# Kernel tuning notes

Measured on AMD Instinct MI355X. Metric: run time of the kernel, lower is better.

The kernel has to match this reference:

```python
import jax, jax.numpy as jnp
import numpy as np

N, IN_F, OUT_F, K = 256, 1024, 128, 32

def setup_inputs() -> dict:
    key = jax.random.key(0)
    k1, k2 = jax.random.split(key)
    x = jax.random.normal(k1, (N, IN_F), dtype=jnp.float32)
    T = jax.random.normal(k2, (IN_F, OUT_F, K), dtype=jnp.float32)
    return {"x": x, "T": T}

def reference(x, T):
    # matrices: [N, OUT_F, K]
    M = jnp.einsum('ni,iok->nok', x, T)
    # pairwise L1 distance over kernel dim: [N, N, OUT_F]
    norm = jnp.abs(M[:, None, :, :] - M[None, :, :, :]).sum(axis=3)
    expnorm = jnp.exp(-norm)
    # sum over the other-sample axis; subtract self-term exp(0)=1
    o_b = expnorm.sum(axis=0) - 1.0  # [N, OUT_F]
    return jnp.concatenate([x, o_b], axis=1)
```

## Files before the change

### kernel.cpp

```cpp
#include <hip/hip_runtime.h>

typedef unsigned short u16;
typedef __attribute__((ext_vector_type(8))) short short8_t;
typedef __attribute__((ext_vector_type(4))) float f32x4;

#define N_SAMP 256
#define IN_F   1024
#define OUT_F  128
#define KDIM   32
#define JTOT   (OUT_F * KDIM)
#define OUT_ROW (IN_F + OUT_F)

#define CHUNKS 8
#define MPC    32
#define MPW    8

__device__ __forceinline__ u16 f2bf(float f) {
    union { float f; unsigned u; } v; v.f = f;
    unsigned r = v.u + 0x7FFFu + ((v.u >> 16) & 1u);
    return (u16)(r >> 16);
}


__global__ __launch_bounds__(256) void copy_init_conv(const float* __restrict__ x,
                                                      float* __restrict__ out,
                                                      u16* __restrict__ At) {
    int n = blockIdx.x, t = threadIdx.x;
    float4 v = reinterpret_cast<const float4*>(x + (size_t)n * IN_F)[t];
    reinterpret_cast<float4*>(out + (size_t)n * OUT_ROW)[t] = v;
    ushort4 b;
    b.x = f2bf(v.x); b.y = f2bf(v.y); b.z = f2bf(v.z); b.w = f2bf(v.w);
    reinterpret_cast<ushort4*>(At + (size_t)n * IN_F)[t] = b;
}

__global__ __launch_bounds__(256) void convT_kernel(const float* __restrict__ T,
                                                    u16* __restrict__ Bt) {
    __shared__ float Ls[64 * 65];
    const int t = threadIdx.x;
    const int j0 = blockIdx.x * 64, k0 = blockIdx.y * 64;
    const int r = t >> 2, c4 = t & 3;

    const float4* src = reinterpret_cast<const float4*>(T + (size_t)(k0 + r) * JTOT + j0 + c4 * 16);
    float4 v0 = src[0], v1 = src[1], v2 = src[2], v3 = src[3];
    float vv[16] = {v0.x,v0.y,v0.z,v0.w, v1.x,v1.y,v1.z,v1.w,
                    v2.x,v2.y,v2.z,v2.w, v3.x,v3.y,v3.z,v3.w};
#pragma unroll
    for (int i = 0; i < 16; ++i) Ls[r * 65 + c4 * 16 + i] = vv[i];
    __syncthreads();

    unsigned pk[8];
#pragma unroll
    for (int i = 0; i < 8; ++i) {
        u16 lo = f2bf(Ls[(c4 * 16 + 2 * i    ) * 65 + r]);
        u16 hi = f2bf(Ls[(c4 * 16 + 2 * i + 1) * 65 + r]);
        pk[i] = (unsigned)lo | ((unsigned)hi << 16);
    }
    uint4* dst = reinterpret_cast<uint4*>(Bt + (size_t)(j0 + r) * IN_F + k0 + c4 * 16);
    dst[0] = make_uint4(pk[0], pk[1], pk[2], pk[3]);
    dst[1] = make_uint4(pk[4], pk[5], pk[6], pk[7]);
}

#define LDB 136
__global__ __launch_bounds__(128) void mfma_gemm(const u16* __restrict__ At,
                                                 const u16* __restrict__ Bt,
                                                 float* __restrict__ Mt) {
    __shared__ u16 Bs[64 * LDB];
    __shared__ u16 As[32 * LDB];
    const int t = threadIdx.x;
    const int w = t >> 6, l = t & 63;
    const int jb = blockIdx.x * 64, nb = blockIdx.y * 32;
    const int rb = t >> 1, hb = t & 1;
    const int ra = t >> 2, qa = t & 3;

    f32x4 acc00 = {0.f,0.f,0.f,0.f}, acc01 = {0.f,0.f,0.f,0.f};
    f32x4 acc10 = {0.f,0.f,0.f,0.f}, acc11 = {0.f,0.f,0.f,0.f};

    float4 sb[8], sa[4];
    auto LOADG = [&](int it) {
        const float4* gb = reinterpret_cast<const float4*>(Bt + (size_t)(jb + rb) * IN_F + it * 128 + hb * 64);
#pragma unroll
        for (int i = 0; i < 8; ++i) sb[i] = gb[i];
        const float4* ga = reinterpret_cast<const float4*>(At + (size_t)(nb + ra) * IN_F + it * 128 + qa * 32);
#pragma unroll
        for (int i = 0; i < 4; ++i) sa[i] = ga[i];
    };
    auto STORE = [&]() {
#pragma unroll
        for (int i = 0; i < 8; ++i) *reinterpret_cast<float4*>(&Bs[rb * LDB + hb * 64 + i * 8]) = sb[i];
#pragma unroll
        for (int i = 0; i < 4; ++i) *reinterpret_cast<float4*>(&As[ra * LDB + qa * 32 + i * 8]) = sa[i];
    };

    LOADG(0); STORE(); __syncthreads();

    for (int it = 0; it < 8; ++it) {
        if (it < 7) LOADG(it + 1);
#pragma unroll
        for (int s = 0; s < 4; ++s) {
            const int co = s * 32 + 8 * (l >> 4);
            short8_t a0 = *reinterpret_cast<const short8_t*>(&Bs[(w * 32 +      (l & 15)) * LDB + co]);
            short8_t a1 = *reinterpret_cast<const short8_t*>(&Bs[(w * 32 + 16 + (l & 15)) * LDB + co]);
            short8_t b0 = *reinterpret_cast<const short8_t*>(&As[(          (l & 15)) * LDB + co]);
            short8_t b1 = *reinterpret_cast<const short8_t*>(&As[(     16 + (l & 15)) * LDB + co]);
            acc00 = __builtin_amdgcn_mfma_f32_16x16x32_bf16(a0, b0, acc00, 0, 0, 0);
            acc01 = __builtin_amdgcn_mfma_f32_16x16x32_bf16(a0, b1, acc01, 0, 0, 0);
            acc10 = __builtin_amdgcn_mfma_f32_16x16x32_bf16(a1, b0, acc10, 0, 0, 0);
            acc11 = __builtin_amdgcn_mfma_f32_16x16x32_bf16(a1, b1, acc11, 0, 0, 0);
        }
        __syncthreads();
        if (it < 7) { STORE(); __syncthreads(); }
    }

    const int jrow = jb + w * 32 + (l >> 4) * 4;
    const int ncol = nb + (l & 15);
#pragma unroll
    for (int r = 0; r < 4; ++r) {
        Mt[(size_t)(jrow + r     ) * N_SAMP + ncol     ] = acc00[r];
        Mt[(size_t)(jrow + r     ) * N_SAMP + ncol + 16] = acc01[r];
        Mt[(size_t)(jrow + 16 + r) * N_SAMP + ncol     ] = acc10[r];
        Mt[(size_t)(jrow + 16 + r) * N_SAMP + ncol + 16] = acc11[r];
    }
}

__global__ __launch_bounds__(256) void dist_part(const float* __restrict__ Mt,
                                                 float* __restrict__ part) {
    __shared__ float Mo[MPC][36];
    __shared__ float Pred[4][N_SAMP];
    const int t = threadIdx.x, w = t >> 6, l = t & 63;
    const int o  = blockIdx.x;
    const int mb = blockIdx.y * MPC;

    {
        const int m = t & 31, kb = (t >> 5) * 4;
#pragma unroll
        for (int kk = 0; kk < 4; ++kk)
            Mo[m][kb + kk] = Mt[(size_t)(o * KDIM + kb + kk) * N_SAMP + mb + m];
    }
    __syncthreads();

    float accd[4][MPW];
#pragma unroll
    for (int r = 0; r < 4; ++r)
#pragma unroll
        for (int m = 0; m < MPW; ++m) accd[r][m] = 0.f;

#pragma unroll
    for (int kh = 0; kh < 4; ++kh) {
        float r0[8], r1[8], r2[8], r3[8];
#pragma unroll
        for (int k = 0; k < 8; ++k) {
            const float* p = Mt + (size_t)(o * KDIM + kh * 8 + k) * N_SAMP + l;
            r0[k] = p[0]; r1[k] = p[64]; r2[k] = p[128]; r3[k] = p[192];
        }
#pragma unroll
        for (int m = 0; m < MPW; ++m) {
            float mo[8];
#pragma unroll
            for (int i = 0; i < 2; ++i)
                *reinterpret_cast<float4*>(&mo[i * 4]) =
                    *reinterpret_cast<const float4*>(&Mo[w * MPW + m][kh * 8 + i * 4]);
#pragma unroll
            for (int k = 0; k < 8; ++k) {
                accd[0][m] += fabsf(r0[k] - mo[k]);
                accd[1][m] += fabsf(r1[k] - mo[k]);
                accd[2][m] += fabsf(r2[k] - mo[k]);
                accd[3][m] += fabsf(r3[k] - mo[k]);
            }
        }
    }

    float a0 = 0.f, a1 = 0.f, a2 = 0.f, a3 = 0.f;
#pragma unroll
    for (int m = 0; m < MPW; ++m) {
        a0 += __expf(-accd[0][m]); a1 += __expf(-accd[1][m]);
        a2 += __expf(-accd[2][m]); a3 += __expf(-accd[3][m]);
    }
    Pred[w][l] = a0; Pred[w][l + 64] = a1; Pred[w][l + 128] = a2; Pred[w][l + 192] = a3;
    __syncthreads();

    {
        float s = Pred[0][t] + Pred[1][t] + Pred[2][t] + Pred[3][t];
        part[(size_t)blockIdx.y * (OUT_F * N_SAMP) + o * N_SAMP + t] = s;
    }
}

__global__ __launch_bounds__(128) void dist_reduce(const float* __restrict__ part,
                                                   float* __restrict__ out) {
    const int n = blockIdx.x, t = threadIdx.x;
    float s = -1.0f;
#pragma unroll
    for (int c = 0; c < CHUNKS; ++c)
        s += part[(size_t)c * (OUT_F * N_SAMP) + t * N_SAMP + n];
    out[(size_t)n * OUT_ROW + IN_F + t] = s;
}

__global__ __launch_bounds__(256) void copy_init_kernel(const float* __restrict__ x,
                                                        float* __restrict__ out) {
    int n = blockIdx.x, t = threadIdx.x;
    reinterpret_cast<float4*>(out + (size_t)n * OUT_ROW)[t] =
        reinterpret_cast<const float4*>(x + (size_t)n * IN_F)[t];
    if (t < OUT_F) out[(size_t)n * OUT_ROW + IN_F + t] = -1.0f;
}

#define BM 64
#define BN 64
#define BK 16
#define AS_STRIDE 68
__global__ __launch_bounds__(256) void gemm_kernel(const float* __restrict__ x,
                                                   const float* __restrict__ T,
                                                   float* __restrict__ M) {
    __shared__ float As_[BK][AS_STRIDE];
    __shared__ float Bs_[BK][BN];
    const int jb = blockIdx.x * BN, nb = blockIdx.y * BM;
    const int t = threadIdx.x, tx = t & 15, ty = t >> 4;
    float acc[4][4] = {};
    for (int k0 = 0; k0 < IN_F; k0 += BK) {
        {
            int row = t >> 2, cg = (t & 3) * 4;
            float4 v = *reinterpret_cast<const float4*>(&x[(size_t)(nb + row) * IN_F + k0 + cg]);
            As_[cg + 0][row] = v.x; As_[cg + 1][row] = v.y;
            As_[cg + 2][row] = v.z; As_[cg + 3][row] = v.w;
        }
        {
            int r = t >> 4, cg = (t & 15) * 4;
            *reinterpret_cast<float4*>(&Bs_[r][cg]) =
                *reinterpret_cast<const float4*>(&T[(size_t)(k0 + r) * JTOT + jb + cg]);
        }
        __syncthreads();
#pragma unroll
        for (int kk = 0; kk < BK; ++kk) {
            float4 av = *reinterpret_cast<const float4*>(&As_[kk][ty * 4]);
            float4 bv = *reinterpret_cast<const float4*>(&Bs_[kk][tx * 4]);
            float a[4] = {av.x, av.y, av.z, av.w}, b[4] = {bv.x, bv.y, bv.z, bv.w};
#pragma unroll
            for (int i = 0; i < 4; ++i)
#pragma unroll
                for (int j = 0; j < 4; ++j) acc[i][j] += a[i] * b[j];
        }
        __syncthreads();
    }
#pragma unroll
    for (int i = 0; i < 4; ++i) {
        int n = nb + ty * 4 + i;
        float4 v = make_float4(acc[i][0], acc[i][1], acc[i][2], acc[i][3]);
        *reinterpret_cast<float4*>(&M[(size_t)n * JTOT + jb + tx * 4]) = v;
    }
}

__global__ __launch_bounds__(256) void dist_kernel(const float* __restrict__ M,
                                                   float* __restrict__ out) {
    __shared__ float Mo_[64][KDIM];
    const int o = blockIdx.x >> 2, chunk = blockIdx.x & 3, t = threadIdx.x;
    float r[KDIM];
    const float4* mrow = reinterpret_cast<const float4*>(&M[(size_t)t * JTOT + o * KDIM]);
#pragma unroll
    for (int f = 0; f < 8; ++f) {
        float4 v = mrow[f];
        r[f*4+0]=v.x; r[f*4+1]=v.y; r[f*4+2]=v.z; r[f*4+3]=v.w;
    }
    const int mbase = chunk * 64;
    {
        int row = t >> 3, f4 = t & 7;
        *reinterpret_cast<float4*>(&Mo_[row][f4*4]) =
            *reinterpret_cast<const float4*>(&M[(size_t)(mbase+row)*JTOT + o*KDIM + f4*4]);
        *reinterpret_cast<float4*>(&Mo_[row+32][f4*4]) =
            *reinterpret_cast<const float4*>(&M[(size_t)(mbase+row+32)*JTOT + o*KDIM + f4*4]);
    }
    __syncthreads();
    float acc = 0.f;
    for (int m = 0; m < 64; ++m) {
        float d = 0.f;
#pragma unroll
        for (int k = 0; k < KDIM; ++k) d += fabsf(r[k] - Mo_[m][k]);
        acc += __expf(-d);
    }
    atomicAdd(&out[(size_t)t * OUT_ROW + IN_F + o], acc);
}

extern "C" void kernel_launch(void* const* d_in, const int* in_sizes, int n_in,
                              void* d_out, int out_size, void* d_ws, size_t ws_size,
                              hipStream_t stream) {
    const float* x = (const float*)d_in[0];
    const float* T = (const float*)d_in[1];
    float* out = (float*)d_out;

    const size_t MT_BYTES = (size_t)JTOT * N_SAMP * 4;
    const size_t AT_BYTES = (size_t)N_SAMP * IN_F * 2;
    const size_t BT_BYTES = (size_t)JTOT * IN_F * 2;

    if (ws_size >= MT_BYTES + AT_BYTES + BT_BYTES) {
        float* Mt = (float*)d_ws;
        u16*   At = (u16*)((char*)d_ws + MT_BYTES);
        u16*   Bt = (u16*)((char*)d_ws + MT_BYTES + AT_BYTES);
        float* part = (float*)Bt;

        copy_init_conv<<<N_SAMP, 256, 0, stream>>>(x, out, At);
        convT_kernel<<<dim3(JTOT / 64, IN_F / 64), 256, 0, stream>>>(T, Bt);
        mfma_gemm<<<dim3(JTOT / 64, N_SAMP / 32), 128, 0, stream>>>(At, Bt, Mt);
        dist_part<<<dim3(OUT_F, CHUNKS), 256, 0, stream>>>(Mt, part);
        dist_reduce<<<N_SAMP, 128, 0, stream>>>(part, out);
    } else {
        float* M = (float*)d_ws;
        copy_init_kernel<<<N_SAMP, 256, 0, stream>>>(x, out);
        dim3 ggrid(JTOT / BN, N_SAMP / BM);
        gemm_kernel<<<ggrid, 256, 0, stream>>>(x, T, M);
        dist_kernel<<<OUT_F * 4, 256, 0, stream>>>(M, out);
    }
}
```

Measured before the change: 120.5 us.

## Fuse GEMM and pairwise L1 distance per output feature into one kernel

Replaces the separate T transpose/convert, MFMA GEMM and distance-partial kernels with one fused kernel per (output feature, half of samples). Each block converts its 32-column slice of T to bf16 on the fly with double buffering, computes all 256 samples' M rows with MFMA, keeps them in shared memory, then computes L1 distances and exp sums directly. This removes the Mt and Bt round trips through global memory and two launches. In exchange the GEMM is computed twice, once per half-block, and A is read straight from global memory without LDS staging. The grid is only 256 blocks of 512 threads, which may limit occupancy.

```diff
diff --git a/kernel.cpp b/kernel.cpp
--- a/kernel.cpp
+++ b/kernel.cpp
@@ -11,20 +11,22 @@
 #define JTOT   (OUT_F * KDIM)
 #define OUT_ROW (IN_F + OUT_F)
 
-#define CHUNKS 8
-#define MPC    32
-#define MPW    8
+#define LDBS 72
+#define LDMS 36
 
 __device__ __forceinline__ u16 f2bf(float f) {
     union { float f; unsigned u; } v; v.f = f;
     unsigned r = v.u + 0x7FFFu + ((v.u >> 16) & 1u);
     return (u16)(r >> 16);
 }
-
-
-__global__ __launch_bounds__(256) void copy_init_conv(const float* __restrict__ x,
-                                                      float* __restrict__ out,
-                                                      u16* __restrict__ At) {
+__device__ __forceinline__ unsigned pack2(float lo, float hi) {
+    return (unsigned)f2bf(lo) | ((unsigned)f2bf(hi) << 16);
+}
+
+
+__global__ __launch_bounds__(256) void conv_x(const float* __restrict__ x,
+                                              float* __restrict__ out,
+                                              u16* __restrict__ At) {
     int n = blockIdx.x, t = threadIdx.x;
     float4 v = reinterpret_cast<const float4*>(x + (size_t)n * IN_F)[t];
     reinterpret_cast<float4*>(out + (size_t)n * OUT_ROW)[t] = v;
@@ -33,165 +35,134 @@
     reinterpret_cast<ushort4*>(At + (size_t)n * IN_F)[t] = b;
 }
 
-__global__ __launch_bounds__(256) void convT_kernel(const float* __restrict__ T,
-                                                    u16* __restrict__ Bt) {
-    __shared__ float Ls[64 * 65];
-    const int t = threadIdx.x;
-    const int j0 = blockIdx.x * 64, k0 = blockIdx.y * 64;
-    const int r = t >> 2, c4 = t & 3;
-
-    const float4* src = reinterpret_cast<const float4*>(T + (size_t)(k0 + r) * JTOT + j0 + c4 * 16);
-    float4 v0 = src[0], v1 = src[1], v2 = src[2], v3 = src[3];
-    float vv[16] = {v0.x,v0.y,v0.z,v0.w, v1.x,v1.y,v1.z,v1.w,
-                    v2.x,v2.y,v2.z,v2.w, v3.x,v3.y,v3.z,v3.w};
-#pragma unroll
-    for (int i = 0; i < 16; ++i) Ls[r * 65 + c4 * 16 + i] = vv[i];
+__global__ __launch_bounds__(512) void fused_od(const u16* __restrict__ At,
+                                                const float* __restrict__ T,
+                                                float* __restrict__ part) {
+    __shared__ u16   Bs[2][32 * LDBS];
+    __shared__ float Ms[N_SAMP * LDMS];
+    __shared__ float Pred[8][N_SAMP];
+    const int t = threadIdx.x, w = t >> 6, l = t & 63;
+    const int o  = blockIdx.x >> 1;
+    const int mh = blockIdx.x & 1;
+    const int jb = o * KDIM;
+
+    const int jt = t & 7, kp = t >> 3;
+    float4 ta, tb;
+    auto LOADT = [&](int c) {
+        if (t < 256) {
+            const int k0 = c * 64;
+            ta = *reinterpret_cast<const float4*>(&T[(size_t)(k0 + 2 * kp    ) * JTOT + jb + jt * 4]);
+            tb = *reinterpret_cast<const float4*>(&T[(size_t)(k0 + 2 * kp + 1) * JTOT + jb + jt * 4]);
+        }
+    };
+    auto STORET = [&](int b) {
+        if (t < 256) {
+            const float* fa = reinterpret_cast<const float*>(&ta);
+            const float* fb = reinterpret_cast<const float*>(&tb);
+#pragma unroll
+            for (int c = 0; c < 4; ++c)
+                *reinterpret_cast<unsigned*>(&Bs[b][(jt * 4 + c) * LDBS + 2 * kp]) = pack2(fa[c], fb[c]);
+        }
+    };
+
+    f32x4 acc[2][2];
+#pragma unroll
+    for (int a = 0; a < 2; ++a)
+#pragma unroll
+        for (int b = 0; b < 2; ++b) acc[a][b] = (f32x4){0.f, 0.f, 0.f, 0.f};
+
+    LOADT(0); STORET(0); __syncthreads();
+
+    for (int c = 0; c < 16; ++c) {
+        const int cur = c & 1;
+        if (c < 15) LOADT(c + 1);
+        const u16* at0 = &At[(size_t)(w * 32 +      (l & 15)) * IN_F + c * 64];
+        const u16* at1 = &At[(size_t)(w * 32 + 16 + (l & 15)) * IN_F + c * 64];
+#pragma unroll
+        for (int s = 0; s < 2; ++s) {
+            const int co = s * 32 + 8 * (l >> 4);
+            short8_t a0 = *reinterpret_cast<const short8_t*>(&Bs[cur][(     (l & 15)) * LDBS + co]);
+            short8_t a1 = *reinterpret_cast<const short8_t*>(&Bs[cur][(16 + (l & 15)) * LDBS + co]);
+            short8_t b0 = *reinterpret_cast<const short8_t*>(&at0[co]);
+            short8_t b1 = *reinterpret_cast<const short8_t*>(&at1[co]);
+            acc[0][0] = __builtin_amdgcn_mfma_f32_16x16x32_bf16(a0, b0, acc[0][0], 0, 0, 0);
+            acc[0][1] = __builtin_amdgcn_mfma_f32_16x16x32_bf16(a0, b1, acc[0][1], 0, 0, 0);
+            acc[1][0] = __builtin_amdgcn_mfma_f32_16x16x32_bf16(a1, b0, acc[1][0], 0, 0, 0);
+            acc[1][1] = __builtin_amdgcn_mfma_f32_16x16x32_bf16(a1, b1, acc[1][1], 0, 0, 0);
+        }
+        if (c < 15) STORET(cur ^ 1);
+        __syncthreads();
+    }
+
+#pragma unroll
+    for (int jt2 = 0; jt2 < 2; ++jt2)
+#pragma unroll
+        for (int nt = 0; nt < 2; ++nt) {
+            const int n  = w * 32 + nt * 16 + (l & 15);
+            const int j0 = jt2 * 16 + (l >> 4) * 4;
+#pragma unroll
+            for (int r = 0; r < 4; ++r)
+                Ms[n * LDMS + j0 + r] = acc[jt2][nt][r];
+        }
     __syncthreads();
 
-    unsigned pk[8];
-#pragma unroll
-    for (int i = 0; i < 8; ++i) {
-        u16 lo = f2bf(Ls[(c4 * 16 + 2 * i    ) * 65 + r]);
-        u16 hi = f2bf(Ls[(c4 * 16 + 2 * i + 1) * 65 + r]);
-        pk[i] = (unsigned)lo | ((unsigned)hi << 16);
-    }
-    uint4* dst = reinterpret_cast<uint4*>(Bt + (size_t)(j0 + r) * IN_F + k0 + c4 * 16);
-    dst[0] = make_uint4(pk[0], pk[1], pk[2], pk[3]);
-    dst[1] = make_uint4(pk[4], pk[5], pk[6], pk[7]);
-}
-
-#define LDB 136
-__global__ __launch_bounds__(128) void mfma_gemm(const u16* __restrict__ At,
-                                                 const u16* __restrict__ Bt,
-                                                 float* __restrict__ Mt) {
-    __shared__ u16 Bs[64 * LDB];
-    __shared__ u16 As[32 * LDB];
-    const int t = threadIdx.x;
-    const int w = t >> 6, l = t & 63;
-    const int jb = blockIdx.x * 64, nb = blockIdx.y * 32;
-    const int rb = t >> 1, hb = t & 1;
-    const int ra = t >> 2, qa = t & 3;
-
-    f32x4 acc00 = {0.f,0.f,0.f,0.f}, acc01 = {0.f,0.f,0.f,0.f};
-    f32x4 acc10 = {0.f,0.f,0.f,0.f}, acc11 = {0.f,0.f,0.f,0.f};
-
-    float4 sb[8], sa[4];
-    auto LOADG = [&](int it) {
-        const float4* gb = reinterpret_cast<const float4*>(Bt + (size_t)(jb + rb) * IN_F + it * 128 + hb * 64);
-#pragma unroll
-        for (int i = 0; i < 8; ++i) sb[i] = gb[i];
-        const float4* ga = reinterpret_cast<const float4*>(At + (size_t)(nb + ra) * IN_F + it * 128 + qa * 32);
-#pragma unroll
-        for (int i = 0; i < 4; ++i) sa[i] = ga[i];
-    };
-    auto STORE = [&]() {
-#pragma unroll
-        for (int i = 0; i < 8; ++i) *reinterpret_cast<float4*>(&Bs[rb * LDB + hb * 64 + i * 8]) = sb[i];
-#pragma unroll
-        for (int i = 0; i < 4; ++i) *reinterpret_cast<float4*>(&As[ra * LDB + qa * 32 + i * 8]) = sa[i];
-    };
-
-    LOADG(0); STORE(); __syncthreads();
-
-    for (int it = 0; it < 8; ++it) {
-        if (it < 7) LOADG(it + 1);
-#pragma unroll
-        for (int s = 0; s < 4; ++s) {
-            const int co = s * 32 + 8 * (l >> 4);
-            short8_t a0 = *reinterpret_cast<const short8_t*>(&Bs[(w * 32 +      (l & 15)) * LDB + co]);
-            short8_t a1 = *reinterpret_cast<const short8_t*>(&Bs[(w * 32 + 16 + (l & 15)) * LDB + co]);
-            short8_t b0 = *reinterpret_cast<const short8_t*>(&As[(          (l & 15)) * LDB + co]);
-            short8_t b1 = *reinterpret_cast<const short8_t*>(&As[(     16 + (l & 15)) * LDB + co]);
-            acc00 = __builtin_amdgcn_mfma_f32_16x16x32_bf16(a0, b0, acc00, 0, 0, 0);
-            acc01 = __builtin_amdgcn_mfma_f32_16x16x32_bf16(a0, b1, acc01, 0, 0, 0);
-            acc10 = __builtin_amdgcn_mfma_f32_16x16x32_bf16(a1, b0, acc10, 0, 0, 0);
-            acc11 = __builtin_amdgcn_mfma_f32_16x16x32_bf16(a1, b1, acc11, 0, 0, 0);
-        }
-        __syncthreads();
-        if (it < 7) { STORE(); __syncthreads(); }
-    }
-
-    const int jrow = jb + w * 32 + (l >> 4) * 4;
-    const int ncol = nb + (l & 15);
-#pragma unroll
-    for (int r = 0; r < 4; ++r) {
-        Mt[(size_t)(jrow + r     ) * N_SAMP + ncol     ] = acc00[r];
-        Mt[(size_t)(jrow + r     ) * N_SAMP + ncol + 16] = acc01[r];
-        Mt[(size_t)(jrow + 16 + r) * N_SAMP + ncol     ] = acc10[r];
-        Mt[(size_t)(jrow + 16 + r) * N_SAMP + ncol + 16] = acc11[r];
-    }
-}
-
-__global__ __launch_bounds__(256) void dist_part(const float* __restrict__ Mt,
-                                                 float* __restrict__ part) {
-    __shared__ float Mo[MPC][36];
-    __shared__ float Pred[4][N_SAMP];
-    const int t = threadIdx.x, w = t >> 6, l = t & 63;
-    const int o  = blockIdx.x;
-    const int mb = blockIdx.y * MPC;
-
-    {
-        const int m = t & 31, kb = (t >> 5) * 4;
-#pragma unroll
-        for (int kk = 0; kk < 4; ++kk)
-            Mo[m][kb + kk] = Mt[(size_t)(o * KDIM + kb + kk) * N_SAMP + mb + m];
-    }
-    __syncthreads();
-
-    float accd[4][MPW];
-#pragma unroll
-    for (int r = 0; r < 4; ++r)
-#pragma unroll
-        for (int m = 0; m < MPW; ++m) accd[r][m] = 0.f;
+    float accd[4][16];
+#pragma unroll
+    for (int ri = 0; ri < 4; ++ri)
+#pragma unroll
+        for (int mi = 0; mi < 16; ++mi) accd[ri][mi] = 0.f;
 
 #pragma unroll
     for (int kh = 0; kh < 4; ++kh) {
-        float r0[8], r1[8], r2[8], r3[8];
-#pragma unroll
-        for (int k = 0; k < 8; ++k) {
-            const float* p = Mt + (size_t)(o * KDIM + kh * 8 + k) * N_SAMP + l;
-            r0[k] = p[0]; r1[k] = p[64]; r2[k] = p[128]; r3[k] = p[192];
-        }
-#pragma unroll
-        for (int m = 0; m < MPW; ++m) {
+        float rr[4][8];
+#pragma unroll
+        for (int ri = 0; ri < 4; ++ri)
+#pragma unroll
+            for (int i = 0; i < 2; ++i)
+                *reinterpret_cast<float4*>(&rr[ri][i * 4]) =
+                    *reinterpret_cast<const float4*>(&Ms[(l + 64 * ri) * LDMS + kh * 8 + i * 4]);
+#pragma unroll
+        for (int mi = 0; mi < 16; ++mi) {
+            const int m = mh * 128 + w * 16 + mi;
             float mo[8];
 #pragma unroll
             for (int i = 0; i < 2; ++i)
                 *reinterpret_cast<float4*>(&mo[i * 4]) =
-                    *reinterpret_cast<const float4*>(&Mo[w * MPW + m][kh * 8 + i * 4]);
+                    *reinterpret_cast<const float4*>(&Ms[m * LDMS + kh * 8 + i * 4]);
 #pragma unroll
             for (int k = 0; k < 8; ++k) {
-                accd[0][m] += fabsf(r0[k] - mo[k]);
-                accd[1][m] += fabsf(r1[k] - mo[k]);
-                accd[2][m] += fabsf(r2[k] - mo[k]);
-                accd[3][m] += fabsf(r3[k] - mo[k]);
+                accd[0][mi] += fabsf(rr[0][k] - mo[k]);
+                accd[1][mi] += fabsf(rr[1][k] - mo[k]);
+                accd[2][mi] += fabsf(rr[2][k] - mo[k]);
+                accd[3][mi] += fabsf(rr[3][k] - mo[k]);
             }
         }
     }
 
-    float a0 = 0.f, a1 = 0.f, a2 = 0.f, a3 = 0.f;
-#pragma unroll
-    for (int m = 0; m < MPW; ++m) {
-        a0 += __expf(-accd[0][m]); a1 += __expf(-accd[1][m]);
-        a2 += __expf(-accd[2][m]); a3 += __expf(-accd[3][m]);
-    }
-    Pred[w][l] = a0; Pred[w][l + 64] = a1; Pred[w][l + 128] = a2; Pred[w][l + 192] = a3;
+    float a[4] = {0.f, 0.f, 0.f, 0.f};
+#pragma unroll
+    for (int mi = 0; mi < 16; ++mi) {
+        a[0] += __expf(-accd[0][mi]); a[1] += __expf(-accd[1][mi]);
+        a[2] += __expf(-accd[2][mi]); a[3] += __expf(-accd[3][mi]);
+    }
+    Pred[w][l] = a[0]; Pred[w][l + 64] = a[1];
+    Pred[w][l + 128] = a[2]; Pred[w][l + 192] = a[3];
     __syncthreads();
 
-    {
-        float s = Pred[0][t] + Pred[1][t] + Pred[2][t] + Pred[3][t];
-        part[(size_t)blockIdx.y * (OUT_F * N_SAMP) + o * N_SAMP + t] = s;
-    }
-}
-
-__global__ __launch_bounds__(128) void dist_reduce(const float* __restrict__ part,
-                                                   float* __restrict__ out) {
-    const int n = blockIdx.x, t = threadIdx.x;
-    float s = -1.0f;
-#pragma unroll
-    for (int c = 0; c < CHUNKS; ++c)
-        s += part[(size_t)c * (OUT_F * N_SAMP) + t * N_SAMP + n];
-    out[(size_t)n * OUT_ROW + IN_F + t] = s;
+    if (t < N_SAMP) {
+        float s = 0.f;
+#pragma unroll
+        for (int ww = 0; ww < 8; ++ww) s += Pred[ww][t];
+        part[(size_t)(mh * OUT_F + o) * N_SAMP + t] = s;
+    }
+}
+
+__global__ __launch_bounds__(128) void reduce2(const float* __restrict__ part,
+                                               float* __restrict__ out) {
+    const int n = blockIdx.x, o = threadIdx.x;
+    float s = part[(size_t)o * N_SAMP + n]
+            + part[(size_t)(OUT_F + o) * N_SAMP + n] - 1.0f;
+    out[(size_t)n * OUT_ROW + IN_F + o] = s;
 }
 
 __global__ __launch_bounds__(256) void copy_init_kernel(const float* __restrict__ x,
@@ -284,21 +255,16 @@
     const float* T = (const float*)d_in[1];
     float* out = (float*)d_out;
 
-    const size_t MT_BYTES = (size_t)JTOT * N_SAMP * 4;
     const size_t AT_BYTES = (size_t)N_SAMP * IN_F * 2;
-    const size_t BT_BYTES = (size_t)JTOT * IN_F * 2;
-
-    if (ws_size >= MT_BYTES + AT_BYTES + BT_BYTES) {
-        float* Mt = (float*)d_ws;
-        u16*   At = (u16*)((char*)d_ws + MT_BYTES);
-        u16*   Bt = (u16*)((char*)d_ws + MT_BYTES + AT_BYTES);
-        float* part = (float*)Bt;
-
-        copy_init_conv<<<N_SAMP, 256, 0, stream>>>(x, out, At);
-        convT_kernel<<<dim3(JTOT / 64, IN_F / 64), 256, 0, stream>>>(T, Bt);
-        mfma_gemm<<<dim3(JTOT / 64, N_SAMP / 32), 128, 0, stream>>>(At, Bt, Mt);
-        dist_part<<<dim3(OUT_F, CHUNKS), 256, 0, stream>>>(Mt, part);
-        dist_reduce<<<N_SAMP, 128, 0, stream>>>(part, out);
+    const size_t NEED = AT_BYTES + (size_t)2 * OUT_F * N_SAMP * 4;
+
+    if (ws_size >= NEED) {
+        u16*   At   = (u16*)d_ws;
+        float* part = (float*)((char*)d_ws + AT_BYTES);
+
+        conv_x<<<N_SAMP, 256, 0, stream>>>(x, out, At);
+        fused_od<<<2 * OUT_F, 512, 0, stream>>>(At, T, part);
+        reduce2<<<N_SAMP, OUT_F, 0, stream>>>(part, out);
     } else {
         float* M = (float*)d_ws;
         copy_init_kernel<<<N_SAMP, 256, 0, stream>>>(x, out);
```

Result: faster. 100.4 us (-16.6%).
